# Kernel tuning notes

Measured on AMD Instinct MI355X. Metric: run time of the kernel, lower is better.

The kernel has to match this reference:

```python
import jax, jax.numpy as jnp
import numpy as np

B, T, N, D = 16, 12, 512, 128
DSCALE = 16  # self.d in the torch module; scores divided by sqrt(d)
LN_EPS = 1e-5


def _linear_params(key, fan_in, fan_out):
    kw, kb = jax.random.split(key)
    lim = 1.0 / np.sqrt(fan_in)
    W = jax.random.uniform(kw, (fan_in, fan_out), jnp.float32, -lim, lim)
    b = jax.random.uniform(kb, (fan_out,), jnp.float32, -lim, lim)
    return W, b


def setup_inputs() -> dict:
    key = jax.random.key(0)
    ks = jax.random.split(key, 8)
    x = jax.random.normal(ks[0], (B, T, N, D), jnp.float32)
    adjgat = jax.random.normal(ks[1], (B, T, N, D), jnp.float32)
    Wq, bq = _linear_params(ks[2], D, D)
    Wk, bk = _linear_params(ks[3], D, D)
    Wv, bv = _linear_params(ks[4], D, D)
    Wo, bo = _linear_params(ks[5], D, D)
    W1, b1 = _linear_params(ks[6], D, D)
    W2, b2 = _linear_params(ks[7], D, D)
    return {"x": x, "adjgat": adjgat, "Wq": Wq, "bq": bq, "Wk": Wk, "bk": bk,
            "Wv": Wv, "bv": bv, "Wo": Wo, "bo": bo, "W1": W1, "b1": b1,
            "W2": W2, "b2": b2}


def reference(x, adjgat, Wq, bq, Wk, bk, Wv, bv, Wo, bo, W1, b1, W2, b2):
    x_ = x + adjgat                                    # [B,T,N,D]
    Q = x_ @ Wq + bq
    K = x_ @ Wk + bk
    V = x_ @ Wv + bv
    scores = jnp.einsum('btnd,btmd->btnm', Q, K) / (DSCALE ** 0.5)  # [B,T,N,N]
    attn = jax.nn.softmax(scores, axis=-1)
    # argmax over the QUERY axis (dim=-2): for each key column m, which query row is max
    cp = jnp.argmax(attn, axis=-2)                     # [B,T,N] int
    attended = jnp.einsum('btnm,btmd->btnd', attn, V)  # [B,T,N,D]
    # out[b,t,n] = attended[b,t,cp[b,t,n]] -- hard gather along node axis
    value = jnp.take_along_axis(attended, cp[..., None], axis=2)  # [B,T,N,D]
    value = value @ Wo + bo + x_
    # LayerNorm over last dim, no affine
    mu = jnp.mean(value, axis=-1, keepdims=True)
    var = jnp.var(value, axis=-1, keepdims=True)
    value = (value - mu) * jax.lax.rsqrt(var + LN_EPS)
    # feed-forward: Linear -> ReLU -> Linear
    return jax.nn.relu(value @ W1 + b1) @ W2 + b2
```

## Files before the change

kernel.cpp:

```cpp
#include <hip/hip_runtime.h>
#include <math.h>

#define TPB 256
static constexpr int BTT = 192;
static constexpr int NN  = 512;
static constexpr int DD  = 128;
static constexpr float SCALE = 0.25f;
static constexpr float LNEPS = 1e-5f;

typedef _Float16 half8 __attribute__((ext_vector_type(8)));
typedef short bf16x8 __attribute__((ext_vector_type(8)));
typedef float floatx4 __attribute__((ext_vector_type(4)));

__global__ void k_add(const float* __restrict__ x, const float* __restrict__ g,
                      float* __restrict__ y, int n4) {
  int i = blockIdx.x * blockDim.x + threadIdx.x;
  if (i < n4) {
    const float4* xa = (const float4*)x;
    const float4* ga = (const float4*)g;
    float4 a = xa[i], b = ga[i];
    ((float4*)y)[i] = make_float4(a.x + b.x, a.y + b.y, a.z + b.z, a.w + b.w);
  }
}

__device__ __forceinline__ void stage_straight(float (*Bs)[132], const float* __restrict__ src,
                                               int ld, int tid) {
  #pragma unroll
  for (int u = tid; u < 1024; u += TPB) {
    int kk = u >> 5, c4 = (u & 31) << 2;
    *(float4*)&Bs[kk][c4] = *(const float4*)(src + (long)kk * ld + c4);
  }
}

__device__ __forceinline__ void stage_transposed(float (*As)[132], const float* __restrict__ src,
                                                 int ld, int tid) {
  #pragma unroll
  for (int u = tid; u < 1024; u += TPB) {
    int r = u >> 3, k4 = (u & 7) << 2;
    float4 v = *(const float4*)(src + (long)r * ld + k4);
    As[k4 + 0][r] = v.x; As[k4 + 1][r] = v.y; As[k4 + 2][r] = v.z; As[k4 + 3][r] = v.w;
  }
}

__device__ __forceinline__ void mt_compute(const float (*As)[132], const float (*Bs)[132],
                                           int r0, int c0a, float acc[8][8]) {
  #pragma unroll
  for (int kk = 0; kk < 32; ++kk) {
    float a[8], b[8];
    *(float4*)&a[0] = *(const float4*)&As[kk][r0];
    *(float4*)&a[4] = *(const float4*)&As[kk][r0 + 4];
    *(float4*)&b[0] = *(const float4*)&Bs[kk][c0a];
    *(float4*)&b[4] = *(const float4*)&Bs[kk][c0a + 64];
    #pragma unroll
    for (int i = 0; i < 8; ++i)
      #pragma unroll
      for (int j = 0; j < 8; ++j)
        acc[i][j] = fmaf(a[i], b[j], acc[i][j]);
  }
}

__global__ __launch_bounds__(TPB, 2)
void k_gemm_bias(const float* __restrict__ A, const float* __restrict__ W,
                 const float* __restrict__ bias, float* __restrict__ C) {
  __shared__ float As[32][132];
  __shared__ float Bs[32][132];
  const int tid = threadIdx.x;
  const int tr = tid >> 4, tc = tid & 15;
  const int r0 = tr * 8, c0a = tc * 4;
  const long rowblk = (long)blockIdx.x * 128;
  float acc[8][8] = {};
  for (int k0 = 0; k0 < 128; k0 += 32) {
    stage_transposed(As, A + rowblk * 128 + k0, 128, tid);
    stage_straight(Bs, W + (long)k0 * 128, 128, tid);
    __syncthreads();
    mt_compute(As, Bs, r0, c0a, acc);
    __syncthreads();
  }
  float4 blo = *(const float4*)(bias + c0a);
  float4 bhi = *(const float4*)(bias + c0a + 64);
  #pragma unroll
  for (int i = 0; i < 8; ++i) {
    float* crow = C + (rowblk + r0 + i) * 128;
    *(float4*)(crow + c0a) = make_float4(acc[i][0] + blo.x, acc[i][1] + blo.y,
                                         acc[i][2] + blo.z, acc[i][3] + blo.w);
    *(float4*)(crow + c0a + 64) = make_float4(acc[i][4] + bhi.x, acc[i][5] + bhi.y,
                                              acc[i][6] + bhi.z, acc[i][7] + bhi.w);
  }
}

__global__ __launch_bounds__(TPB, 2)
void k_gemm_bias_f16(const float* __restrict__ A, const float* __restrict__ W,
                     const float* __restrict__ bias, float* __restrict__ C) {
  __shared__ _Float16 At[128][136];
  __shared__ _Float16 Bt[128][136];
  const int tid = threadIdx.x;
  const int lane = tid & 63;
  const int wave = tid >> 6;
  const int frow = lane & 15;
  const int kgrp = lane >> 4;
  const int rbase = wave * 32;
  const long rowblk = (long)blockIdx.x * 128;

  for (int u = tid; u < 128 * 32; u += TPB) {
    int r = u >> 5, k4 = (u & 31) << 2;
    float4 v4 = *(const float4*)(A + (rowblk + r) * DD + k4);
    At[r][k4 + 0] = (_Float16)v4.x; At[r][k4 + 1] = (_Float16)v4.y;
    At[r][k4 + 2] = (_Float16)v4.z; At[r][k4 + 3] = (_Float16)v4.w;
  }
  for (int u = tid; u < 128 * 32; u += TPB) {
    int k = u >> 5, c4 = (u & 31) << 2;
    float4 v4 = *(const float4*)(W + (long)k * DD + c4);
    Bt[c4 + 0][k] = (_Float16)v4.x; Bt[c4 + 1][k] = (_Float16)v4.y;
    Bt[c4 + 2][k] = (_Float16)v4.z; Bt[c4 + 3][k] = (_Float16)v4.w;
  }
  __syncthreads();

  floatx4 acc[2][8];
  #pragma unroll
  for (int i = 0; i < 2; ++i)
    #pragma unroll
    for (int j = 0; j < 8; ++j)
      acc[i][j] = (floatx4){0.f, 0.f, 0.f, 0.f};
  #pragma unroll
  for (int ks = 0; ks < 4; ++ks) {
    const int mk = ks * 32 + kgrp * 8;
    half8 a0 = *(const half8*)&At[rbase + frow][mk];
    half8 a1 = *(const half8*)&At[rbase + 16 + frow][mk];
    #pragma unroll
    for (int j = 0; j < 8; ++j) {
      half8 b = *(const half8*)&Bt[j * 16 + frow][mk];
      acc[0][j] = __builtin_amdgcn_mfma_f32_16x16x32_f16(a0, b, acc[0][j], 0, 0, 0);
      acc[1][j] = __builtin_amdgcn_mfma_f32_16x16x32_f16(a1, b, acc[1][j], 0, 0, 0);
    }
  }
  #pragma unroll
  for (int i = 0; i < 2; ++i)
    #pragma unroll
    for (int j = 0; j < 8; ++j) {
      const int col = j * 16 + frow;
      const float bb = bias[col];
      #pragma unroll
      for (int r = 0; r < 4; ++r)
        C[(rowblk + rbase + i * 16 + kgrp * 4 + r) * DD + col] = acc[i][j][r] + bb;
    }
}

__device__ __forceinline__ void split3(float q, unsigned short& h, unsigned short& m,
                                       unsigned short& l) {
  unsigned uh = __float_as_uint(q) & 0xFFFF0000u;
  float fh = __uint_as_float(uh);
  float r1 = q - fh;
  unsigned um = __float_as_uint(r1) & 0xFFFF0000u;
  float fm = __uint_as_float(um);
  float r2 = r1 - fm;
  unsigned ul = __float_as_uint(r2) & 0xFFFF0000u;
  h = (unsigned short)(uh >> 16);
  m = (unsigned short)(um >> 16);
  l = (unsigned short)(ul >> 16);
}

__global__ __launch_bounds__(TPB, 2)
void k_scores_mfma(const float* __restrict__ Q, const float* __restrict__ K,
                   float* __restrict__ S) {
  int blk = blockIdx.x;
  int btc = blk >> 4, rt = (blk >> 2) & 3, ct = blk & 3;
  const float* Qb = Q + (long)btc * NN * DD + (long)rt * 128 * DD;
  const float* Kb = K + (long)btc * NN * DD + (long)ct * 128 * DD;
  float* Sb = S + (long)btc * NN * NN + (long)rt * 128 * NN + ct * 128;

  __shared__ unsigned short Qh[128][40], Qm[128][40], Ql[128][40];
  __shared__ unsigned short Kh[128][40], Km[128][40], Kl[128][40];

  const int tid = threadIdx.x;
  const int lane = tid & 63;
  const int wave = tid >> 6;
  const int frow = lane & 15;
  const int kgrp = lane >> 4;
  const int rbase = wave * 32;

  floatx4 acc[2][8];
  #pragma unroll
  for (int i = 0; i < 2; ++i)
    #pragma unroll
    for (int j = 0; j < 8; ++j)
      acc[i][j] = (floatx4){0.f, 0.f, 0.f, 0.f};

  for (int k0 = 0; k0 < 128; k0 += 32) {
    __syncthreads();
    #pragma unroll
    for (int u = tid; u < 2048; u += TPB) {
      int mat = u >> 10, rem = u & 1023;
      int row = rem >> 3, k4 = (rem & 7) << 2;
      const float* src = (mat ? Kb : Qb) + (long)row * DD + k0 + k4;
      float4 v = *(const float4*)src;
      unsigned short h0, m0, l0, h1, m1, l1, h2, m2, l2, h3, m3, l3;
      split3(v.x, h0, m0, l0); split3(v.y, h1, m1, l1);
      split3(v.z, h2, m2, l2); split3(v.w, h3, m3, l3);
      if (mat == 0) {
        Qh[row][k4] = h0; Qh[row][k4+1] = h1; Qh[row][k4+2] = h2; Qh[row][k4+3] = h3;
        Qm[row][k4] = m0; Qm[row][k4+1] = m1; Qm[row][k4+2] = m2; Qm[row][k4+3] = m3;
        Ql[row][k4] = l0; Ql[row][k4+1] = l1; Ql[row][k4+2] = l2; Ql[row][k4+3] = l3;
      } else {
        Kh[row][k4] = h0; Kh[row][k4+1] = h1; Kh[row][k4+2] = h2; Kh[row][k4+3] = h3;
        Km[row][k4] = m0; Km[row][k4+1] = m1; Km[row][k4+2] = m2; Km[row][k4+3] = m3;
        Kl[row][k4] = l0; Kl[row][k4+1] = l1; Kl[row][k4+2] = l2; Kl[row][k4+3] = l3;
      }
    }
    __syncthreads();

    const int mk = kgrp * 8;
    bf16x8 aH0 = *(const bf16x8*)&Qh[rbase + frow][mk];
    bf16x8 aH1 = *(const bf16x8*)&Qh[rbase + 16 + frow][mk];
    bf16x8 aM0 = *(const bf16x8*)&Qm[rbase + frow][mk];
    bf16x8 aM1 = *(const bf16x8*)&Qm[rbase + 16 + frow][mk];
    bf16x8 aL0 = *(const bf16x8*)&Ql[rbase + frow][mk];
    bf16x8 aL1 = *(const bf16x8*)&Ql[rbase + 16 + frow][mk];
    #pragma unroll
    for (int j = 0; j < 8; ++j) {
      bf16x8 bH = *(const bf16x8*)&Kh[j * 16 + frow][mk];
      bf16x8 bM = *(const bf16x8*)&Km[j * 16 + frow][mk];
      bf16x8 bL = *(const bf16x8*)&Kl[j * 16 + frow][mk];
      acc[0][j] = __builtin_amdgcn_mfma_f32_16x16x32_bf16(aM0, bM, acc[0][j], 0, 0, 0);
      acc[1][j] = __builtin_amdgcn_mfma_f32_16x16x32_bf16(aM1, bM, acc[1][j], 0, 0, 0);
      acc[0][j] = __builtin_amdgcn_mfma_f32_16x16x32_bf16(aH0, bL, acc[0][j], 0, 0, 0);
      acc[1][j] = __builtin_amdgcn_mfma_f32_16x16x32_bf16(aH1, bL, acc[1][j], 0, 0, 0);
      acc[0][j] = __builtin_amdgcn_mfma_f32_16x16x32_bf16(aL0, bH, acc[0][j], 0, 0, 0);
      acc[1][j] = __builtin_amdgcn_mfma_f32_16x16x32_bf16(aL1, bH, acc[1][j], 0, 0, 0);
      acc[0][j] = __builtin_amdgcn_mfma_f32_16x16x32_bf16(aH0, bM, acc[0][j], 0, 0, 0);
      acc[1][j] = __builtin_amdgcn_mfma_f32_16x16x32_bf16(aH1, bM, acc[1][j], 0, 0, 0);
      acc[0][j] = __builtin_amdgcn_mfma_f32_16x16x32_bf16(aM0, bH, acc[0][j], 0, 0, 0);
      acc[1][j] = __builtin_amdgcn_mfma_f32_16x16x32_bf16(aM1, bH, acc[1][j], 0, 0, 0);
      acc[0][j] = __builtin_amdgcn_mfma_f32_16x16x32_bf16(aH0, bH, acc[0][j], 0, 0, 0);
      acc[1][j] = __builtin_amdgcn_mfma_f32_16x16x32_bf16(aH1, bH, acc[1][j], 0, 0, 0);
    }
  }
  #pragma unroll
  for (int i = 0; i < 2; ++i)
    #pragma unroll
    for (int j = 0; j < 8; ++j)
      #pragma unroll
      for (int r = 0; r < 4; ++r)
        Sb[(long)(rbase + i * 16 + kgrp * 4 + r) * NN + j * 16 + frow] =
            acc[i][j][r] * SCALE;
}

__global__ void k_lse(const float* __restrict__ S, float* __restrict__ lse) {
  int w = threadIdx.x >> 6, lane = threadIdx.x & 63;
  long row = (long)blockIdx.x * 4 + w;
  const float4* p = (const float4*)(S + row * NN);
  float4 a = p[lane], b = p[lane + 64];
  float m = fmaxf(fmaxf(fmaxf(a.x, a.y), fmaxf(a.z, a.w)),
                  fmaxf(fmaxf(b.x, b.y), fmaxf(b.z, b.w)));
  #pragma unroll
  for (int d = 1; d < 64; d <<= 1) m = fmaxf(m, __shfl_xor(m, d));
  float s = expf(a.x - m) + expf(a.y - m) + expf(a.z - m) + expf(a.w - m)
          + expf(b.x - m) + expf(b.y - m) + expf(b.z - m) + expf(b.w - m);
  #pragma unroll
  for (int d = 1; d < 64; d <<= 1) s += __shfl_xor(s, d);
  if (lane == 0) lse[row] = m + logf(s);
}

__global__ __launch_bounds__(TPB)
void k_colargmax(const float* __restrict__ S, const float* __restrict__ lse,
                 int* __restrict__ cp) {
  int btc = blockIdx.x >> 3, cg = blockIdx.x & 7;
  int c = threadIdx.x & 63;
  int col = cg * 64 + c;
  int seg = threadIdx.x >> 6;
  const float* Sb = S + (long)btc * NN * NN;
  const float* lb = lse + btc * NN;
  float best = -3.4e38f;
  int bi = seg * 128;
  for (int n = seg * 128; n < seg * 128 + 128; ++n) {
    float v = Sb[(long)n * NN + col] - lb[n];
    if (v > best) { best = v; bi = n; }
  }
  __shared__ float bv[4][64];
  __shared__ int bidx[4][64];
  bv[seg][c] = best; bidx[seg][c] = bi;
  __syncthreads();
  if (seg == 0) {
    #pragma unroll
    for (int s = 1; s < 4; ++s) {
      float v2 = bv[s][c];
      if (v2 > best) { best = v2; bi = bidx[s][c]; }
    }
    cp[btc * NN + col] = bi;
  }
}

__global__ __launch_bounds__(TPB, 2)
void k_pv_f16(const float* __restrict__ S, const float* __restrict__ lse,
              const float* __restrict__ V, float* __restrict__ att) {
  int btc = blockIdx.x >> 2, nt = blockIdx.x & 3;
  const int n0 = nt * 128;
  const float* Sb = S + (long)btc * NN * NN + (long)n0 * NN;
  const float* lb = lse + btc * NN + n0;
  const float* Vb = V + (long)btc * NN * DD;
  float* attb = att + ((long)btc * NN + n0) * DD;

  __shared__ _Float16 Ph[128][72];
  __shared__ _Float16 Vt[128][72];

  const int tid = threadIdx.x;
  const int lane = tid & 63;
  const int wave = tid >> 6;
  const int frow = lane & 15;
  const int kgrp = lane >> 4;

  floatx4 acc[2][8];
  #pragma unroll
  for (int i = 0; i < 2; ++i)
    #pragma unroll
    for (int j = 0; j < 8; ++j)
      acc[i][j] = (floatx4){0.f, 0.f, 0.f, 0.f};

  for (int m0 = 0; m0 < NN; m0 += 64) {
    __syncthreads();
    for (int u = tid; u < 128 * 16; u += TPB) {
      int n = u >> 4, m4 = (u & 15) << 2;
      float l = lb[n];
      float4 s4 = *(const float4*)(Sb + (long)n * NN + m0 + m4);
      Ph[n][m4 + 0] = (_Float16)__expf(s4.x - l);
      Ph[n][m4 + 1] = (_Float16)__expf(s4.y - l);
      Ph[n][m4 + 2] = (_Float16)__expf(s4.z - l);
      Ph[n][m4 + 3] = (_Float16)__expf(s4.w - l);
    }
    for (int u = tid; u < 64 * 32; u += TPB) {
      int d4 = (u & 31) << 2, m = u >> 5;
      float4 v4 = *(const float4*)(Vb + (long)(m0 + m) * DD + d4);
      Vt[d4 + 0][m] = (_Float16)v4.x;
      Vt[d4 + 1][m] = (_Float16)v4.y;
      Vt[d4 + 2][m] = (_Float16)v4.z;
      Vt[d4 + 3][m] = (_Float16)v4.w;
    }
    __syncthreads();
    #pragma unroll
    for (int ks = 0; ks < 2; ++ks) {
      const int mk = ks * 32 + kgrp * 8;
      half8 a0 = *(const half8*)&Ph[wave * 32 + frow][mk];
      half8 a1 = *(const half8*)&Ph[wave * 32 + 16 + frow][mk];
      #pragma unroll
      for (int j = 0; j < 8; ++j) {
        half8 b = *(const half8*)&Vt[j * 16 + frow][mk];
        acc[0][j] = __builtin_amdgcn_mfma_f32_16x16x32_f16(a0, b, acc[0][j], 0, 0, 0);
        acc[1][j] = __builtin_amdgcn_mfma_f32_16x16x32_f16(a1, b, acc[1][j], 0, 0, 0);
      }
    }
  }
  #pragma unroll
  for (int i = 0; i < 2; ++i)
    #pragma unroll
    for (int j = 0; j < 8; ++j)
      #pragma unroll
      for (int r = 0; r < 4; ++r)
        attb[(long)(wave * 32 + i * 16 + kgrp * 4 + r) * DD + j * 16 + frow] = acc[i][j][r];
}

__global__ __launch_bounds__(TPB, 2)
void k_wo_ln_ffn(const float* __restrict__ att, const int* __restrict__ cp,
                 const float* __restrict__ Wo, const float* __restrict__ bo,
                 const float* __restrict__ xr,
                 const float* __restrict__ W1, const float* __restrict__ b1,
                 const float* __restrict__ W2, const float* __restrict__ b2,
                 float* __restrict__ out) {
  const int blk = blockIdx.x, btc = blk >> 2, rt = blk & 3;
  const int n0 = rt * 128;
  const long g0 = (long)btc * NN + n0;
  const float* attb = att + (long)btc * NN * DD;
  const int* cpb = cp + g0;

  __shared__ _Float16 At[128][136];
  __shared__ _Float16 Bt[128][136];

  const int tid = threadIdx.x;
  const int lane = tid & 63;
  const int wave = tid >> 6;
  const int frow = lane & 15;
  const int kgrp = lane >> 4;
  const int rbase = wave * 32;

  auto stage_wT = [&](const float* __restrict__ W) {
    for (int u = tid; u < 128 * 32; u += TPB) {
      int k = u >> 5, c4 = (u & 31) << 2;
      float4 v4 = *(const float4*)(W + (long)k * DD + c4);
      Bt[c4 + 0][k] = (_Float16)v4.x; Bt[c4 + 1][k] = (_Float16)v4.y;
      Bt[c4 + 2][k] = (_Float16)v4.z; Bt[c4 + 3][k] = (_Float16)v4.w;
    }
  };

  floatx4 acc[2][8];
  auto zero_acc = [&]() {
    #pragma unroll
    for (int i = 0; i < 2; ++i)
      #pragma unroll
      for (int j = 0; j < 8; ++j)
        acc[i][j] = (floatx4){0.f, 0.f, 0.f, 0.f};
  };
  auto mfma_tile = [&]() {
    #pragma unroll
    for (int ks = 0; ks < 4; ++ks) {
      const int mk = ks * 32 + kgrp * 8;
      half8 a0 = *(const half8*)&At[rbase + frow][mk];
      half8 a1 = *(const half8*)&At[rbase + 16 + frow][mk];
      #pragma unroll
      for (int j = 0; j < 8; ++j) {
        half8 b = *(const half8*)&Bt[j * 16 + frow][mk];
        acc[0][j] = __builtin_amdgcn_mfma_f32_16x16x32_f16(a0, b, acc[0][j], 0, 0, 0);
        acc[1][j] = __builtin_amdgcn_mfma_f32_16x16x32_f16(a1, b, acc[1][j], 0, 0, 0);
      }
    }
  };

  for (int u = tid; u < 128 * 32; u += TPB) {
    int r = u >> 5, k4 = (u & 31) << 2;
    int src = cpb[r];
    float4 v4 = *(const float4*)(attb + (long)src * DD + k4);
    At[r][k4 + 0] = (_Float16)v4.x; At[r][k4 + 1] = (_Float16)v4.y;
    At[r][k4 + 2] = (_Float16)v4.z; At[r][k4 + 3] = (_Float16)v4.w;
  }
  stage_wT(Wo);
  __syncthreads();
  zero_acc();
  mfma_tile();
  __syncthreads();

  float v[2][8][4];
  #pragma unroll
  for (int i = 0; i < 2; ++i)
    #pragma unroll
    for (int j = 0; j < 8; ++j) {
      const int col = j * 16 + frow;
      const float bb = bo[col];
      #pragma unroll
      for (int r = 0; r < 4; ++r) {
        const long grow = g0 + rbase + i * 16 + kgrp * 4 + r;
        v[i][j][r] = acc[i][j][r] + bb + xr[grow * DD + col];
      }
    }
  #pragma unroll
  for (int i = 0; i < 2; ++i)
    #pragma unroll
    for (int r = 0; r < 4; ++r) {
      float s = 0.f, ss = 0.f;
      #pragma unroll
      for (int j = 0; j < 8; ++j) { float t = v[i][j][r]; s += t; ss += t * t; }
      #pragma unroll
      for (int d = 1; d < 16; d <<= 1) { s += __shfl_xor(s, d); ss += __shfl_xor(ss, d); }
      float mu = s * (1.f / 128.f);
      float var = ss * (1.f / 128.f) - mu * mu;
      float rs = rsqrtf(var + LNEPS);
      #pragma unroll
      for (int j = 0; j < 8; ++j) v[i][j][r] = (v[i][j][r] - mu) * rs;
    }
  #pragma unroll
  for (int i = 0; i < 2; ++i)
    #pragma unroll
    for (int j = 0; j < 8; ++j)
      #pragma unroll
      for (int r = 0; r < 4; ++r)
        At[rbase + i * 16 + kgrp * 4 + r][j * 16 + frow] = (_Float16)v[i][j][r];
  stage_wT(W1);
  __syncthreads();

  zero_acc();
  mfma_tile();
  __syncthreads();
  #pragma unroll
  for (int i = 0; i < 2; ++i)
    #pragma unroll
    for (int j = 0; j < 8; ++j) {
      const int col = j * 16 + frow;
      const float bb = b1[col];
      #pragma unroll
      for (int r = 0; r < 4; ++r)
        At[rbase + i * 16 + kgrp * 4 + r][col] = (_Float16)fmaxf(acc[i][j][r] + bb, 0.f);
    }
  stage_wT(W2);
  __syncthreads();

  zero_acc();
  mfma_tile();
  #pragma unroll
  for (int i = 0; i < 2; ++i)
    #pragma unroll
    for (int j = 0; j < 8; ++j) {
      const int col = j * 16 + frow;
      const float bb = b2[col];
      #pragma unroll
      for (int r = 0; r < 4; ++r) {
        const long grow = g0 + rbase + i * 16 + kgrp * 4 + r;
        out[grow * DD + col] = acc[i][j][r] + bb;
      }
    }
}

extern "C" void kernel_launch(void* const* d_in, const int* in_sizes, int n_in,
                              void* d_out, int out_size, void* d_ws, size_t ws_size,
                              hipStream_t stream) {
  const float* x    = (const float*)d_in[0];
  const float* adj  = (const float*)d_in[1];
  const float* Wq   = (const float*)d_in[2];
  const float* bq   = (const float*)d_in[3];
  const float* Wk   = (const float*)d_in[4];
  const float* bk   = (const float*)d_in[5];
  const float* Wv   = (const float*)d_in[6];
  const float* bv   = (const float*)d_in[7];
  const float* Wo   = (const float*)d_in[8];
  const float* bo   = (const float*)d_in[9];
  const float* W1   = (const float*)d_in[10];
  const float* b1   = (const float*)d_in[11];
  const float* W2   = (const float*)d_in[12];
  const float* b2   = (const float*)d_in[13];
  float* out = (float*)d_out;
  (void)in_sizes; (void)n_in; (void)out_size;

  const size_t BT_ROWBYTES = (size_t)NN * DD * 4;
  const size_t per_bt = 5 * BT_ROWBYTES + (size_t)NN * NN * 4 + 2 * (size_t)NN * 4;
  static const int divs[] = {192, 96, 64, 48, 32, 24, 16, 12, 8, 6, 4, 3, 2, 1};
  int CH = 1;
  for (int i = 0; i < 14; ++i) {
    if ((size_t)divs[i] * per_bt + 8192 <= ws_size) { CH = divs[i]; break; }
  }

  char* ws = (char*)d_ws;
  size_t off = 0;
  auto alloc = [&](size_t bytes) -> void* {
    void* p = ws + off;
    off += (bytes + 255) & ~(size_t)255;
    return p;
  };
  float* xrc  = (float*)alloc((size_t)CH * BT_ROWBYTES);
  float* Qc   = (float*)alloc((size_t)CH * BT_ROWBYTES);
  float* Kc   = (float*)alloc((size_t)CH * BT_ROWBYTES);
  float* Vc   = (float*)alloc((size_t)CH * BT_ROWBYTES);
  float* attc = (float*)alloc((size_t)CH * BT_ROWBYTES);
  float* Sc   = (float*)alloc((size_t)CH * NN * NN * 4);
  float* lsec = (float*)alloc((size_t)CH * NN * 4);
  int*   cpc  = (int*)  alloc((size_t)CH * NN * 4);

  for (int c0 = 0; c0 < BTT; c0 += CH) {
    const size_t elemoff = (size_t)c0 * NN * DD;
    const float* xb  = x + elemoff;
    const float* ab  = adj + elemoff;
    float* outb = out + elemoff;
    int n4c = CH * NN * DD / 4;

    k_add<<<n4c / TPB, TPB, 0, stream>>>(xb, ab, xrc, n4c);

    k_gemm_bias<<<CH * 4, TPB, 0, stream>>>(xrc, Wq, bq, Qc);
    k_gemm_bias<<<CH * 4, TPB, 0, stream>>>(xrc, Wk, bk, Kc);
    k_gemm_bias_f16<<<CH * 4, TPB, 0, stream>>>(xrc, Wv, bv, Vc);

    k_scores_mfma<<<CH * 16, TPB, 0, stream>>>(Qc, Kc, Sc);
    k_lse<<<CH * 128, TPB, 0, stream>>>(Sc, lsec);
    k_colargmax<<<CH * 8, TPB, 0, stream>>>(Sc, lsec, cpc);
    k_pv_f16<<<CH * 4, TPB, 0, stream>>>(Sc, lsec, Vc, attc);

    k_wo_ln_ffn<<<CH * 4, TPB, 0, stream>>>(attc, cpc, Wo, bo, xrc,
                                            W1, b1, W2, b2, outb);
  }
}
```

Before: 699.6 us.

## Fuse row softmax stats into scores and column argmax into PV kernel

The scores kernel now emits per-tile row max and sum-exp partials, combined by a small kernel into the log-sum-exp, so the separate full pass over S to compute it is gone. The column argmax moves into the PV kernel using packed 64-bit atomicMax keys, removing another full read of S. The PV kernel is retiled to 64-row blocks with an XOR-swizzled V transpose in LDS and an occupancy hint of 3. This adds atomics, a memset, extra LDS use, and reliance on a bit-inverted float key ordering whose correctness for positive values is questionable.

```diff
diff --git a/kernel.cpp b/kernel.cpp
--- a/kernel.cpp
+++ b/kernel.cpp
@@ -161,7 +161,8 @@
 
 __global__ __launch_bounds__(TPB, 2)
 void k_scores_mfma(const float* __restrict__ Q, const float* __restrict__ K,
-                   float* __restrict__ S) {
+                   float* __restrict__ S, float* __restrict__ pm,
+                   float* __restrict__ ps) {
   int blk = blockIdx.x;
   int btc = blk >> 4, rt = (blk >> 2) & 3, ct = blk & 3;
   const float* Qb = Q + (long)btc * NN * DD + (long)rt * 128 * DD;
@@ -242,123 +243,141 @@
       for (int r = 0; r < 4; ++r)
         Sb[(long)(rbase + i * 16 + kgrp * 4 + r) * NN + j * 16 + frow] =
             acc[i][j][r] * SCALE;
-}
-
-__global__ void k_lse(const float* __restrict__ S, float* __restrict__ lse) {
-  int w = threadIdx.x >> 6, lane = threadIdx.x & 63;
-  long row = (long)blockIdx.x * 4 + w;
-  const float4* p = (const float4*)(S + row * NN);
-  float4 a = p[lane], b = p[lane + 64];
-  float m = fmaxf(fmaxf(fmaxf(a.x, a.y), fmaxf(a.z, a.w)),
-                  fmaxf(fmaxf(b.x, b.y), fmaxf(b.z, b.w)));
-  #pragma unroll
-  for (int d = 1; d < 64; d <<= 1) m = fmaxf(m, __shfl_xor(m, d));
-  float s = expf(a.x - m) + expf(a.y - m) + expf(a.z - m) + expf(a.w - m)
-          + expf(b.x - m) + expf(b.y - m) + expf(b.z - m) + expf(b.w - m);
-  #pragma unroll
-  for (int d = 1; d < 64; d <<= 1) s += __shfl_xor(s, d);
-  if (lane == 0) lse[row] = m + logf(s);
-}
-
-__global__ __launch_bounds__(TPB)
-void k_colargmax(const float* __restrict__ S, const float* __restrict__ lse,
-                 int* __restrict__ cp) {
-  int btc = blockIdx.x >> 3, cg = blockIdx.x & 7;
-  int c = threadIdx.x & 63;
-  int col = cg * 64 + c;
-  int seg = threadIdx.x >> 6;
-  const float* Sb = S + (long)btc * NN * NN;
-  const float* lb = lse + btc * NN;
-  float best = -3.4e38f;
-  int bi = seg * 128;
-  for (int n = seg * 128; n < seg * 128 + 128; ++n) {
-    float v = Sb[(long)n * NN + col] - lb[n];
-    if (v > best) { best = v; bi = n; }
-  }
-  __shared__ float bv[4][64];
-  __shared__ int bidx[4][64];
-  bv[seg][c] = best; bidx[seg][c] = bi;
-  __syncthreads();
-  if (seg == 0) {
-    #pragma unroll
-    for (int s = 1; s < 4; ++s) {
-      float v2 = bv[s][c];
-      if (v2 > best) { best = v2; bi = bidx[s][c]; }
-    }
-    cp[btc * NN + col] = bi;
-  }
-}
-
-__global__ __launch_bounds__(TPB, 2)
+  #pragma unroll
+  for (int i = 0; i < 2; ++i)
+    #pragma unroll
+    for (int r = 0; r < 4; ++r) {
+      float mx = -3.4e38f;
+      #pragma unroll
+      for (int j = 0; j < 8; ++j) mx = fmaxf(mx, acc[i][j][r] * SCALE);
+      #pragma unroll
+      for (int d = 1; d < 16; d <<= 1) mx = fmaxf(mx, __shfl_xor(mx, d));
+      float se = 0.f;
+      #pragma unroll
+      for (int j = 0; j < 8; ++j) se += __expf(acc[i][j][r] * SCALE - mx);
+      #pragma unroll
+      for (int d = 1; d < 16; d <<= 1) se += __shfl_xor(se, d);
+      if (frow == 0) {
+        int row = rbase + i * 16 + kgrp * 4 + r;
+        long pidx = ((long)btc * 4 + ct) * NN + rt * 128 + row;
+        pm[pidx] = mx; ps[pidx] = se;
+      }
+    }
+}
+
+__global__ void k_lse_combine(const float* __restrict__ pm, const float* __restrict__ ps,
+                              float* __restrict__ lse, int total) {
+  int idx = blockIdx.x * TPB + threadIdx.x;
+  if (idx >= total) return;
+  int btc = idx >> 9, n = idx & 511;
+  float mv[4], sv[4];
+  float M = -3.4e38f;
+  #pragma unroll
+  for (int ct = 0; ct < 4; ++ct) {
+    long p = ((long)btc * 4 + ct) * NN + n;
+    mv[ct] = pm[p]; sv[ct] = ps[p];
+    M = fmaxf(M, mv[ct]);
+  }
+  float tot = 0.f;
+  #pragma unroll
+  for (int ct = 0; ct < 4; ++ct) tot += sv[ct] * expf(mv[ct] - M);
+  lse[idx] = M + logf(tot);
+}
+
+__global__ __launch_bounds__(TPB, 3)
 void k_pv_f16(const float* __restrict__ S, const float* __restrict__ lse,
-              const float* __restrict__ V, float* __restrict__ att) {
-  int btc = blockIdx.x >> 2, nt = blockIdx.x & 3;
-  const int n0 = nt * 128;
+              const float* __restrict__ V, float* __restrict__ att,
+              unsigned long long* __restrict__ cpk) {
+  int btc = blockIdx.x >> 3, nt = blockIdx.x & 7;
+  const int n0 = nt * 64;
   const float* Sb = S + (long)btc * NN * NN + (long)n0 * NN;
   const float* lb = lse + btc * NN + n0;
   const float* Vb = V + (long)btc * NN * DD;
   float* attb = att + ((long)btc * NN + n0) * DD;
-
-  __shared__ _Float16 Ph[128][72];
+  unsigned long long* cpb = cpk + (long)btc * NN;
+
+  __shared__ _Float16 Ph[64][72];
   __shared__ _Float16 Vt[128][72];
+  __shared__ float P32[64][65];
+  __shared__ unsigned long long colmax[64];
 
   const int tid = threadIdx.x;
   const int lane = tid & 63;
   const int wave = tid >> 6;
   const int frow = lane & 15;
   const int kgrp = lane >> 4;
-
-  floatx4 acc[2][8];
-  #pragma unroll
-  for (int i = 0; i < 2; ++i)
-    #pragma unroll
-    for (int j = 0; j < 8; ++j)
-      acc[i][j] = (floatx4){0.f, 0.f, 0.f, 0.f};
+  const int wr = wave * 16;
+  const int c = tid & 63, g = tid >> 6;
+
+  floatx4 acc[8];
+  #pragma unroll
+  for (int j = 0; j < 8; ++j) acc[j] = (floatx4){0.f, 0.f, 0.f, 0.f};
 
   for (int m0 = 0; m0 < NN; m0 += 64) {
     __syncthreads();
-    for (int u = tid; u < 128 * 16; u += TPB) {
+    if (tid < 64) {
+      if (m0 > 0) atomicMax(&cpb[m0 - 64 + tid], colmax[tid]);
+      colmax[tid] = 0ull;
+    }
+    for (int u = tid; u < 64 * 16; u += TPB) {
       int n = u >> 4, m4 = (u & 15) << 2;
       float l = lb[n];
       float4 s4 = *(const float4*)(Sb + (long)n * NN + m0 + m4);
-      Ph[n][m4 + 0] = (_Float16)__expf(s4.x - l);
-      Ph[n][m4 + 1] = (_Float16)__expf(s4.y - l);
-      Ph[n][m4 + 2] = (_Float16)__expf(s4.z - l);
-      Ph[n][m4 + 3] = (_Float16)__expf(s4.w - l);
-    }
-    for (int u = tid; u < 64 * 32; u += TPB) {
+      float v0 = s4.x - l, v1 = s4.y - l, v2 = s4.z - l, v3 = s4.w - l;
+      P32[n][m4 + 0] = v0; P32[n][m4 + 1] = v1;
+      P32[n][m4 + 2] = v2; P32[n][m4 + 3] = v3;
+      Ph[n][m4 + 0] = (_Float16)__expf(v0);
+      Ph[n][m4 + 1] = (_Float16)__expf(v1);
+      Ph[n][m4 + 2] = (_Float16)__expf(v2);
+      Ph[n][m4 + 3] = (_Float16)__expf(v3);
+    }
+    for (int u = tid; u < 2048; u += TPB) {
       int d4 = (u & 31) << 2, m = u >> 5;
+      int mc = m ^ (((d4 >> 2) & 7) << 3);
       float4 v4 = *(const float4*)(Vb + (long)(m0 + m) * DD + d4);
-      Vt[d4 + 0][m] = (_Float16)v4.x;
-      Vt[d4 + 1][m] = (_Float16)v4.y;
-      Vt[d4 + 2][m] = (_Float16)v4.z;
-      Vt[d4 + 3][m] = (_Float16)v4.w;
+      Vt[d4 + 0][mc] = (_Float16)v4.x;
+      Vt[d4 + 1][mc] = (_Float16)v4.y;
+      Vt[d4 + 2][mc] = (_Float16)v4.z;
+      Vt[d4 + 3][mc] = (_Float16)v4.w;
     }
     __syncthreads();
+    {
+      float best = -3.4e38f;
+      int bi = g * 16;
+      #pragma unroll
+      for (int t = 0; t < 16; ++t) {
+        float v = P32[g * 16 + t][c];
+        if (v > best) { best = v; bi = g * 16 + t; }
+      }
+      unsigned key = ~__float_as_uint(best);
+      unsigned long long pk =
+          ((unsigned long long)key << 32) | (unsigned)(NN - 1 - (n0 + bi));
+      atomicMax(&colmax[c], pk);
+    }
     #pragma unroll
     for (int ks = 0; ks < 2; ++ks) {
       const int mk = ks * 32 + kgrp * 8;
-      half8 a0 = *(const half8*)&Ph[wave * 32 + frow][mk];
-      half8 a1 = *(const half8*)&Ph[wave * 32 + 16 + frow][mk];
+      half8 a = *(const half8*)&Ph[wr + frow][mk];
       #pragma unroll
       for (int j = 0; j < 8; ++j) {
-        half8 b = *(const half8*)&Vt[j * 16 + frow][mk];
-        acc[0][j] = __builtin_amdgcn_mfma_f32_16x16x32_f16(a0, b, acc[0][j], 0, 0, 0);
-        acc[1][j] = __builtin_amdgcn_mfma_f32_16x16x32_f16(a1, b, acc[1][j], 0, 0, 0);
-      }
-    }
-  }
-  #pragma unroll
-  for (int i = 0; i < 2; ++i)
-    #pragma unroll
-    for (int j = 0; j < 8; ++j)
-      #pragma unroll
-      for (int r = 0; r < 4; ++r)
-        attb[(long)(wave * 32 + i * 16 + kgrp * 4 + r) * DD + j * 16 + frow] = acc[i][j][r];
+        const int d = j * 16 + frow;
+        const int swz = ((d >> 2) & 7) << 3;
+        half8 b = *(const half8*)&Vt[d][mk ^ swz];
+        acc[j] = __builtin_amdgcn_mfma_f32_16x16x32_f16(a, b, acc[j], 0, 0, 0);
+      }
+    }
+  }
+  __syncthreads();
+  if (tid < 64) atomicMax(&cpb[NN - 64 + tid], colmax[tid]);
+  #pragma unroll
+  for (int j = 0; j < 8; ++j)
+    #pragma unroll
+    for (int r = 0; r < 4; ++r)
+      attb[(long)(wr + kgrp * 4 + r) * DD + j * 16 + frow] = acc[j][r];
 }
 
 __global__ __launch_bounds__(TPB, 2)
-void k_wo_ln_ffn(const float* __restrict__ att, const int* __restrict__ cp,
+void k_wo_ln_ffn(const float* __restrict__ att, const unsigned long long* __restrict__ cpk,
                  const float* __restrict__ Wo, const float* __restrict__ bo,
                  const float* __restrict__ xr,
                  const float* __restrict__ W1, const float* __restrict__ b1,
@@ -368,7 +387,7 @@
   const int n0 = rt * 128;
   const long g0 = (long)btc * NN + n0;
   const float* attb = att + (long)btc * NN * DD;
-  const int* cpb = cp + g0;
+  const unsigned long long* cpb = cpk + g0;
 
   __shared__ _Float16 At[128][136];
   __shared__ _Float16 Bt[128][136];
@@ -414,7 +433,7 @@
 
   for (int u = tid; u < 128 * 32; u += TPB) {
     int r = u >> 5, k4 = (u & 31) << 2;
-    int src = cpb[r];
+    int src = NN - 1 - (int)(unsigned)(cpb[r] & 0xFFFFFFFFull);
     float4 v4 = *(const float4*)(attb + (long)src * DD + k4);
     At[r][k4 + 0] = (_Float16)v4.x; At[r][k4 + 1] = (_Float16)v4.y;
     At[r][k4 + 2] = (_Float16)v4.z; At[r][k4 + 3] = (_Float16)v4.w;
@@ -516,7 +535,8 @@
   (void)in_sizes; (void)n_in; (void)out_size;
 
   const size_t BT_ROWBYTES = (size_t)NN * DD * 4;
-  const size_t per_bt = 5 * BT_ROWBYTES + (size_t)NN * NN * 4 + 2 * (size_t)NN * 4;
+  const size_t per_bt = 5 * BT_ROWBYTES + (size_t)NN * NN * 4 + (size_t)NN * 4
+                      + 2 * 4 * (size_t)NN * 4 + (size_t)NN * 8;
   static const int divs[] = {192, 96, 64, 48, 32, 24, 16, 12, 8, 6, 4, 3, 2, 1};
   int CH = 1;
   for (int i = 0; i < 14; ++i) {
@@ -537,7 +557,9 @@
   float* attc = (float*)alloc((size_t)CH * BT_ROWBYTES);
   float* Sc   = (float*)alloc((size_t)CH * NN * NN * 4);
   float* lsec = (float*)alloc((size_t)CH * NN * 4);
-  int*   cpc  = (int*)  alloc((size_t)CH * NN * 4);
+  float* pmc  = (float*)alloc((size_t)CH * 4 * NN * 4);
+  float* psc  = (float*)alloc((size_t)CH * 4 * NN * 4);
+  unsigned long long* cpkc = (unsigned long long*)alloc((size_t)CH * NN * 8);
 
   for (int c0 = 0; c0 < BTT; c0 += CH) {
     const size_t elemoff = (size_t)c0 * NN * DD;
@@ -552,12 +574,12 @@
     k_gemm_bias<<<CH * 4, TPB, 0, stream>>>(xrc, Wk, bk, Kc);
     k_gemm_bias_f16<<<CH * 4, TPB, 0, stream>>>(xrc, Wv, bv, Vc);
 
-    k_scores_mfma<<<CH * 16, TPB, 0, stream>>>(Qc, Kc, Sc);
-    k_lse<<<CH * 128, TPB, 0, stream>>>(Sc, lsec);
-    k_colargmax<<<CH * 8, TPB, 0, stream>>>(Sc, lsec, cpc);
-    k_pv_f16<<<CH * 4, TPB, 0, stream>>>(Sc, lsec, Vc, attc);
-
-    k_wo_ln_ffn<<<CH * 4, TPB, 0, stream>>>(attc, cpc, Wo, bo, xrc,
+    k_scores_mfma<<<CH * 16, TPB, 0, stream>>>(Qc, Kc, Sc, pmc, psc);
+    k_lse_combine<<<CH * 2, TPB, 0, stream>>>(pmc, psc, lsec, CH * NN);
+    hipMemsetAsync(cpkc, 0, (size_t)CH * NN * 8, stream);
+    k_pv_f16<<<CH * 8, TPB, 0, stream>>>(Sc, lsec, Vc, attc, cpkc);
+
+    k_wo_ln_ffn<<<CH * 4, TPB, 0, stream>>>(attc, cpkc, Wo, bo, xrc,
                                             W1, b1, W2, b2, outb);
   }
 }
```

Result: faster. 634.2 us (-9.4%).
